# Kernel tuning notes

Hardware: AMD Instinct MI355X
Metric: run time of the kernel (lower is better)

Reference implementation:

```python
import jax, jax.numpy as jnp
import numpy as np

B, C, D = 32, 24, 12          # batch, feature channels, spatial grid
Q_DIM = 11                    # hardcoded question dim in original (k*2+11)
K = C + 2                     # channels after coordinate concat
G_IN = 2 * K + Q_DIM          # 63
G_HID = 256
F_OUT = 10


def setup_inputs() -> dict:
    key = jax.random.key(0)
    ks = jax.random.split(key, 7)
    s = lambda fan_in: 1.0 / np.sqrt(fan_in)
    return {
        "image": jax.random.normal(ks[0], (B, C, D, D), jnp.float32),
        "question": jax.random.normal(ks[1], (B, Q_DIM), jnp.float32),
        "Wg1": jax.random.normal(ks[2], (G_IN, G_HID), jnp.float32) * s(G_IN),
        "bg1": jnp.zeros((G_HID,), jnp.float32),
        "Wg2": jax.random.normal(ks[3], (G_HID, G_HID), jnp.float32) * s(G_HID),
        "bg2": jnp.zeros((G_HID,), jnp.float32),
        "Wf1": jax.random.normal(ks[4], (G_HID, G_HID), jnp.float32) * s(G_HID),
        "bf1": jnp.zeros((G_HID,), jnp.float32),
        "Wf2": jax.random.normal(ks[5], (G_HID, F_OUT), jnp.float32) * s(G_HID),
        "bf2": jnp.zeros((F_OUT,), jnp.float32),
    }


def reference(image, question, Wg1, bg1, Wg2, bg2, Wf1, bf1, Wf2, bf2):
    b, c, d, _ = image.shape
    # coordinate channels: torch.arange(0, 1+1e-5, 1/(d-1)) == linspace(0,1,d)
    coord = jnp.linspace(0.0, 1.0, d, dtype=image.dtype)
    cx = jnp.broadcast_to(coord[None, None, None, :], (b, 1, d, d))
    cy = jnp.broadcast_to(coord[None, None, :, None], (b, 1, d, d))
    x = jnp.concatenate([image, cx, cy], axis=1)            # [b, k, d, d]
    k = c + 2
    n = d * d
    x = x.reshape(b, k, n).transpose(0, 2, 1)                # [b, n, k] objects
    # all-pairs construction: left repeats objects along axis 1, right along axis 2
    x_left = jnp.broadcast_to(x[:, None, :, :], (b, n, n, k)).reshape(b, n * n, k)
    x_right = jnp.broadcast_to(x[:, :, None, :], (b, n, n, k)).reshape(b, n * n, k)
    q = jnp.broadcast_to(question[:, None, :], (b, n * n, question.shape[1]))
    pairs = jnp.concatenate([x_left, x_right, q], axis=2)    # [b, n^2, 2k+11]
    # shared MLP g per pair
    h = jax.nn.relu(jnp.einsum('bpi,ih->bph', pairs, Wg1) + bg1)
    h = jax.nn.relu(jnp.einsum('bph,ho->bpo', h, Wg2) + bg2)
    s = h.sum(axis=1)                                        # [b, 256] sum over pairs
    # MLP f
    o = jax.nn.relu(s @ Wf1 + bf1)
    return o @ Wf2 + bf2                                     # [b, 10]
```

## Files before the change

kernel.cpp:

```cpp
#include <hip/hip_runtime.h>
#include <hip/hip_bf16.h>

#define NB   32
#define NC   24
#define ND   12
#define NN   144
#define QD   11
#define GH   256
#define FOUT 10

typedef unsigned short u16;
typedef __attribute__((ext_vector_type(8))) short bf16x8;
typedef __attribute__((ext_vector_type(4))) float f32x4;

#define LQ_U16  0
#define R_U16   1179648
#define BS_U16  2359296
#define S_BYTE  4849664

__device__ inline float b2f(u16 v) {
  union { unsigned u; float f; } c; c.u = ((unsigned)v) << 16; return c.f;
}
__device__ inline u16 f2b(float f) {
  __hip_bfloat16 h = __float2bfloat16(f);
  return *reinterpret_cast<u16*>(&h);
}

__global__ __launch_bounds__(256) void prep(const float* __restrict__ image,
                                            const float* __restrict__ question,
                                            const float* __restrict__ Wg1,
                                            const float* __restrict__ bg1,
                                            const float* __restrict__ Wg2,
                                            u16* __restrict__ Lq,
                                            u16* __restrict__ R,
                                            float* __restrict__ S,
                                            u16* __restrict__ Bswz) {
  int blk = blockIdx.x;
  int h   = threadIdx.x;
  if (blk < 256) {
    const int quarter = blk & 3;
    const int b       = (blk >> 2) & 31;
    const int which   = blk >> 7;
    float Wl[NC + 2];
#pragma unroll
    for (int r = 0; r < NC + 2; ++r)
      Wl[r] = Wg1[(which * (NC + 2) + r) * GH + h];
    float qacc = 0.f;
    if (which == 0) {
      qacc = bg1[h];
#pragma unroll
      for (int tq = 0; tq < QD; ++tq)
        qacc += question[b * QD + tq] * Wg1[(2 * (NC + 2) + tq) * GH + h];
    }
    const float* img = image + b * (NC * NN);
    u16* dst = (which == 0 ? Lq : R) + b * NN * GH + h;
    const float inv = 1.0f / (ND - 1);
#pragma unroll 4
    for (int p = quarter * 36; p < quarter * 36 + 36; ++p) {
      float acc = qacc;
#pragma unroll
      for (int c = 0; c < NC; ++c) acc += img[c * NN + p] * Wl[c];
      int i = p / ND, j = p - i * ND;
      acc += (j * inv) * Wl[24];
      acc += (i * inv) * Wl[25];
      dst[p * GH] = f2b(acc);
    }
  } else {
    int tid = (blk - 256) * 256 + h;
    int e   = tid & 7;
    int l   = (tid >> 3) & 63;
    int fid = tid >> 9;
    int kt  = fid >> 4, nt = fid & 15;
    int k = kt * 32 + ((l >> 4) << 3) + e;
    int n = (nt << 4) + (l & 15);
    Bswz[tid] = f2b(Wg2[k * GH + n]);
    if (tid < NB * GH) S[tid] = 0.f;
  }
}

__global__ __launch_bounds__(512, 2) void pair_gemm(const u16* __restrict__ Lq,
                                                    const u16* __restrict__ R,
                                                    const u16* __restrict__ Bswz,
                                                    const float* __restrict__ bg2,
                                                    float* __restrict__ S) {
  const int bid = blockIdx.x;
  const int xcd = bid & 7;
  const int idx = bid >> 3;
  const int b   = xcd * 4 + (idx >> 4);
  const int bi  = idx & 15;
  const int t0  = bi * 10 + (bi < 2 ? bi : 2);
  const int cnt = 10 + (bi < 2 ? 1 : 0);

  if (idx & 32) __builtin_amdgcn_s_sleep(94);

  __shared__ __align__(16) u16 As[8 * 8 * 64 * 8];

  const int t = threadIdx.x;
  const int w = t >> 6, l = t & 63;
  const int wn = w & 3, wm = w >> 2;
  const int brow = t >> 2;
  const int oc   = t & 3;
  const int mf_w   = brow >> 4;
  const int lane_w = ((brow & 15) | (oc << 4)) ^ (oc << 1);
  const int lane_r = l ^ (((l >> 4) & 3) << 1);

  const u16* Lbase = Lq + b * NN * GH;
  const u16* Rbase = R + b * NN * GH;
  const u16* Bl    = Bswz + l * 8;

  float bgv[4];
#pragma unroll
  for (int nt = 0; nt < 4; ++nt)
    bgv[nt] = bg2[(wn << 6) + (nt << 4) + (l & 15)];
  float ssum[4] = {0.f, 0.f, 0.f, 0.f};

  for (int tt = 0; tt < cnt; ++tt) {
    {
      int p = (t0 + tt) * 128 + brow;
      int i = p / NN, j = p - i * NN;
      const u16* Lr = Lbase + i * GH + oc * 8;
      const u16* Rr = Rbase + j * GH + oc * 8;
#pragma unroll
      for (int half = 0; half < 2; ++half) {
        bf16x8 lv[4], rv[4];
#pragma unroll
        for (int q = 0; q < 4; ++q) {
          lv[q] = *(const bf16x8*)(Lr + ((half << 2) | q) * 32);
          rv[q] = *(const bf16x8*)(Rr + ((half << 2) | q) * 32);
        }
#pragma unroll
        for (int q = 0; q < 4; ++q) {
          const int kt = (half << 2) | q;
          u16 o[8];
#pragma unroll
          for (int e = 0; e < 8; ++e) {
            float v = b2f((u16)lv[q][e]) + b2f((u16)rv[q][e]);
            o[e] = f2b(v > 0.f ? v : 0.f);
          }
          *(bf16x8*)&As[((((kt << 3) | mf_w) << 6) | lane_w) << 3] =
              *(bf16x8*)o;
        }
      }
    }
    __syncthreads();

    f32x4 acc[4][4] = {};
#pragma unroll
    for (int kt = 0; kt < 8; ++kt) {
      bf16x8 af[4];
#pragma unroll
      for (int mf = 0; mf < 4; ++mf)
        af[mf] = *(const bf16x8*)
            &As[((((kt << 3) | (wm << 2) | mf) << 6) | lane_r) << 3];
      bf16x8 bfr[4];
#pragma unroll
      for (int nt = 0; nt < 4; ++nt) {
        int fid = (kt << 4) | (wn << 2) | nt;
        bfr[nt] = *(const bf16x8*)(Bl + ((size_t)fid << 9));
      }
      __builtin_amdgcn_s_setprio(1);
#pragma unroll
      for (int mf = 0; mf < 4; ++mf)
#pragma unroll
        for (int nt = 0; nt < 4; ++nt)
          acc[mf][nt] = __builtin_amdgcn_mfma_f32_16x16x32_bf16(
              af[mf], bfr[nt], acc[mf][nt], 0, 0, 0);
      __builtin_amdgcn_s_setprio(0);
    }
#pragma unroll
    for (int nt = 0; nt < 4; ++nt) {
      float s = 0.f;
#pragma unroll
      for (int mf = 0; mf < 4; ++mf)
#pragma unroll
        for (int r = 0; r < 4; ++r) {
          float v = acc[mf][nt][r] + bgv[nt];
          s += v > 0.f ? v : 0.f;
        }
      ssum[nt] += s;
    }
    __syncthreads();
  }

  float* Sb = S + b * GH;
#pragma unroll
  for (int nt = 0; nt < 4; ++nt) {
    float s = ssum[nt];
    s += __shfl_xor(s, 16, 64);
    s += __shfl_xor(s, 32, 64);
    if (l < 16) atomicAdd(&Sb[(wn << 6) + (nt << 4) + l], s);
  }
}

__global__ __launch_bounds__(256) void final_mlp(const float* __restrict__ S,
                                                 const float* __restrict__ Wf1,
                                                 const float* __restrict__ bf1,
                                                 const float* __restrict__ Wf2,
                                                 const float* __restrict__ bf2,
                                                 float* __restrict__ out) {
  __shared__ float sS[GH];
  __shared__ float oS[GH];
  int b = blockIdx.x, h = threadIdx.x;
  sS[h] = S[b * GH + h];
  __syncthreads();
  float acc = bf1[h];
#pragma unroll 8
  for (int k = 0; k < GH; ++k) acc += sS[k] * Wf1[k * GH + h];
  oS[h] = acc > 0.f ? acc : 0.f;
  __syncthreads();
  if (h < FOUT) {
    float o = bf2[h];
#pragma unroll 8
    for (int k = 0; k < GH; ++k) o += oS[k] * Wf2[k * FOUT + h];
    out[b * FOUT + h] = o;
  }
}

extern "C" void kernel_launch(void* const* d_in, const int* in_sizes, int n_in,
                              void* d_out, int out_size, void* d_ws, size_t ws_size,
                              hipStream_t stream) {
  const float* image    = (const float*)d_in[0];
  const float* question = (const float*)d_in[1];
  const float* Wg1      = (const float*)d_in[2];
  const float* bg1      = (const float*)d_in[3];
  const float* Wg2      = (const float*)d_in[4];
  const float* bg2      = (const float*)d_in[5];
  const float* Wf1      = (const float*)d_in[6];
  const float* bf1      = (const float*)d_in[7];
  const float* Wf2      = (const float*)d_in[8];
  const float* bf2      = (const float*)d_in[9];
  float* out = (float*)d_out;

  u16*   wsb  = (u16*)d_ws;
  u16*   Lqp  = wsb + LQ_U16;
  u16*   Rp   = wsb + R_U16;
  u16*   Bswz = wsb + BS_U16;
  float* Sp   = (float*)((char*)d_ws + S_BYTE);

  prep<<<512, 256, 0, stream>>>(image, question, Wg1, bg1, Wg2,
                                Lqp, Rp, Sp, Bswz);
  pair_gemm<<<512, 512, 0, stream>>>(Lqp, Rp, Bswz, bg2, Sp);
  final_mlp<<<NB, 256, 0, stream>>>(Sp, Wf1, bf1, Wf2, bf2, out);
}
```

Baseline: 110.6 us.

## Warp-specialize pair GEMM into producer and MFMA consumer waves with double-buffered LDS

Splits each block into four producer waves and four consumer waves. The producers build the relu(L+R) A tile into a double-buffered LDS buffer while the consumers run MFMA on the other buffer, each consumer covering 128 rows by 64 columns. The grid is halved to 256 blocks with twice the tiles per block, and the sleep staggering and priority hints are removed. The aim is to overlap A-tile construction with matrix math. The trade-off is fewer resident blocks, doubled LDS per block, and only half the waves issuing MFMA.

```diff
diff --git a/kernel.cpp b/kernel.cpp
--- a/kernel.cpp
+++ b/kernel.cpp
@@ -78,7 +78,7 @@
   }
 }
 
-__global__ __launch_bounds__(512, 2) void pair_gemm(const u16* __restrict__ Lq,
+__global__ __launch_bounds__(512, 1) void pair_gemm(const u16* __restrict__ Lq,
                                                     const u16* __restrict__ R,
                                                     const u16* __restrict__ Bswz,
                                                     const float* __restrict__ bg2,
@@ -86,109 +86,133 @@
   const int bid = blockIdx.x;
   const int xcd = bid & 7;
   const int idx = bid >> 3;
-  const int b   = xcd * 4 + (idx >> 4);
-  const int bi  = idx & 15;
-  const int t0  = bi * 10 + (bi < 2 ? bi : 2);
-  const int cnt = 10 + (bi < 2 ? 1 : 0);
-
-  if (idx & 32) __builtin_amdgcn_s_sleep(94);
-
-  __shared__ __align__(16) u16 As[8 * 8 * 64 * 8];
+  const int b   = xcd * 4 + (idx >> 3);
+  const int bi  = idx & 7;
+  const int t0  = bi * 20 + (bi < 2 ? bi : 2);
+  const int cnt = 20 + (bi < 2 ? 1 : 0);
+
+  __shared__ __align__(16) u16 As[2][32768];
 
   const int t = threadIdx.x;
   const int w = t >> 6, l = t & 63;
-  const int wn = w & 3, wm = w >> 2;
-  const int brow = t >> 2;
-  const int oc   = t & 3;
-  const int mf_w   = brow >> 4;
-  const int lane_w = ((brow & 15) | (oc << 4)) ^ (oc << 1);
-  const int lane_r = l ^ (((l >> 4) & 3) << 1);
 
   const u16* Lbase = Lq + b * NN * GH;
   const u16* Rbase = R + b * NN * GH;
-  const u16* Bl    = Bswz + l * 8;
-
-  float bgv[4];
-#pragma unroll
-  for (int nt = 0; nt < 4; ++nt)
-    bgv[nt] = bg2[(wn << 6) + (nt << 4) + (l & 15)];
-  float ssum[4] = {0.f, 0.f, 0.f, 0.f};
-
-  for (int tt = 0; tt < cnt; ++tt) {
+
+  if (w >= 4) {
+    const int tl    = t & 255;
+    const int row   = tl >> 1;
+    const int khalf = tl & 1;
+    const int mf_w  = row >> 4;
+
     {
-      int p = (t0 + tt) * 128 + brow;
+      int p = t0 * 128 + row;
       int i = p / NN, j = p - i * NN;
-      const u16* Lr = Lbase + i * GH + oc * 8;
-      const u16* Rr = Rbase + j * GH + oc * 8;
-#pragma unroll
-      for (int half = 0; half < 2; ++half) {
-        bf16x8 lv[4], rv[4];
-#pragma unroll
-        for (int q = 0; q < 4; ++q) {
-          lv[q] = *(const bf16x8*)(Lr + ((half << 2) | q) * 32);
-          rv[q] = *(const bf16x8*)(Rr + ((half << 2) | q) * 32);
-        }
-#pragma unroll
-        for (int q = 0; q < 4; ++q) {
-          const int kt = (half << 2) | q;
+      const u16* Lr = Lbase + i * GH + khalf * 128;
+      const u16* Rr = Rbase + j * GH + khalf * 128;
+#pragma unroll
+      for (int u = 0; u < 16; ++u) {
+        bf16x8 lv = *(const bf16x8*)(Lr + u * 8);
+        bf16x8 rv = *(const bf16x8*)(Rr + u * 8);
+        u16 o[8];
+#pragma unroll
+        for (int e = 0; e < 8; ++e) {
+          float v = b2f((u16)lv[e]) + b2f((u16)rv[e]);
+          o[e] = f2b(v > 0.f ? v : 0.f);
+        }
+        const int kt = (khalf << 2) + (u >> 2);
+        const int oc = u & 3;
+        const int lw = ((row & 15) | (oc << 4)) ^ (oc << 1);
+        *(bf16x8*)&As[0][((((kt << 3) | mf_w) << 6) | lw) << 3] = *(bf16x8*)o;
+      }
+    }
+    __syncthreads();
+
+    int cur = 0;
+    for (int tt = 0; tt < cnt; ++tt) {
+      if (tt + 1 < cnt) {
+        int p = (t0 + tt + 1) * 128 + row;
+        int i = p / NN, j = p - i * NN;
+        const u16* Lr = Lbase + i * GH + khalf * 128;
+        const u16* Rr = Rbase + j * GH + khalf * 128;
+        u16* dst = &As[cur ^ 1][0];
+#pragma unroll
+        for (int u = 0; u < 16; ++u) {
+          bf16x8 lv = *(const bf16x8*)(Lr + u * 8);
+          bf16x8 rv = *(const bf16x8*)(Rr + u * 8);
           u16 o[8];
 #pragma unroll
           for (int e = 0; e < 8; ++e) {
-            float v = b2f((u16)lv[q][e]) + b2f((u16)rv[q][e]);
+            float v = b2f((u16)lv[e]) + b2f((u16)rv[e]);
             o[e] = f2b(v > 0.f ? v : 0.f);
           }
-          *(bf16x8*)&As[((((kt << 3) | mf_w) << 6) | lane_w) << 3] =
-              *(bf16x8*)o;
-        }
-      }
-    }
+          const int kt = (khalf << 2) + (u >> 2);
+          const int oc = u & 3;
+          const int lw = ((row & 15) | (oc << 4)) ^ (oc << 1);
+          *(bf16x8*)&dst[((((kt << 3) | mf_w) << 6) | lw) << 3] = *(bf16x8*)o;
+        }
+      }
+      __syncthreads();
+      cur ^= 1;
+    }
+  } else {
+    const int lane_r = l ^ (((l >> 4) & 3) << 1);
+    const u16* Bl = Bswz + l * 8;
+
+    float bgv[4];
+#pragma unroll
+    for (int nt = 0; nt < 4; ++nt)
+      bgv[nt] = bg2[(w << 6) + (nt << 4) + (l & 15)];
+    float ssum[4] = {0.f, 0.f, 0.f, 0.f};
+
     __syncthreads();
 
-    f32x4 acc[4][4] = {};
-#pragma unroll
-    for (int kt = 0; kt < 8; ++kt) {
-      bf16x8 af[4];
-#pragma unroll
-      for (int mf = 0; mf < 4; ++mf)
-        af[mf] = *(const bf16x8*)
-            &As[((((kt << 3) | (wm << 2) | mf) << 6) | lane_r) << 3];
-      bf16x8 bfr[4];
+    int cur = 0;
+    for (int tt = 0; tt < cnt; ++tt) {
+      const u16* src = &As[cur][0];
+      f32x4 acc[8][4] = {};
+#pragma unroll
+      for (int kt = 0; kt < 8; ++kt) {
+        bf16x8 bfr[4];
+#pragma unroll
+        for (int nt = 0; nt < 4; ++nt) {
+          int fid = (kt << 4) | (w << 2) | nt;
+          bfr[nt] = *(const bf16x8*)(Bl + ((size_t)fid << 9));
+        }
+#pragma unroll
+        for (int mf = 0; mf < 8; ++mf) {
+          bf16x8 af = *(const bf16x8*)
+              &src[((((kt << 3) | mf) << 6) | lane_r) << 3];
+#pragma unroll
+          for (int nt = 0; nt < 4; ++nt)
+            acc[mf][nt] = __builtin_amdgcn_mfma_f32_16x16x32_bf16(
+                af, bfr[nt], acc[mf][nt], 0, 0, 0);
+        }
+      }
 #pragma unroll
       for (int nt = 0; nt < 4; ++nt) {
-        int fid = (kt << 4) | (wn << 2) | nt;
-        bfr[nt] = *(const bf16x8*)(Bl + ((size_t)fid << 9));
-      }
-      __builtin_amdgcn_s_setprio(1);
-#pragma unroll
-      for (int mf = 0; mf < 4; ++mf)
-#pragma unroll
-        for (int nt = 0; nt < 4; ++nt)
-          acc[mf][nt] = __builtin_amdgcn_mfma_f32_16x16x32_bf16(
-              af[mf], bfr[nt], acc[mf][nt], 0, 0, 0);
-      __builtin_amdgcn_s_setprio(0);
-    }
+        float s = 0.f;
+#pragma unroll
+        for (int mf = 0; mf < 8; ++mf)
+#pragma unroll
+          for (int r = 0; r < 4; ++r) {
+            float v = acc[mf][nt][r] + bgv[nt];
+            s += v > 0.f ? v : 0.f;
+          }
+        ssum[nt] += s;
+      }
+      __syncthreads();
+      cur ^= 1;
+    }
+
+    float* Sb = S + b * GH;
 #pragma unroll
     for (int nt = 0; nt < 4; ++nt) {
-      float s = 0.f;
-#pragma unroll
-      for (int mf = 0; mf < 4; ++mf)
-#pragma unroll
-        for (int r = 0; r < 4; ++r) {
-          float v = acc[mf][nt][r] + bgv[nt];
-          s += v > 0.f ? v : 0.f;
-        }
-      ssum[nt] += s;
-    }
-    __syncthreads();
-  }
-
-  float* Sb = S + b * GH;
-#pragma unroll
-  for (int nt = 0; nt < 4; ++nt) {
-    float s = ssum[nt];
-    s += __shfl_xor(s, 16, 64);
-    s += __shfl_xor(s, 32, 64);
-    if (l < 16) atomicAdd(&Sb[(wn << 6) + (nt << 4) + l], s);
+      float s = ssum[nt];
+      s += __shfl_xor(s, 16, 64);
+      s += __shfl_xor(s, 32, 64);
+      if (l < 16) atomicAdd(&Sb[(w << 6) + (nt << 4) + l], s);
+    }
   }
 }
 
@@ -239,6 +263,6 @@
 
   prep<<<512, 256, 0, stream>>>(image, question, Wg1, bg1, Wg2,
                                 Lqp, Rp, Sp, Bswz);
-  pair_gemm<<<512, 512, 0, stream>>>(Lqp, Rp, Bswz, bg2, Sp);
+  pair_gemm<<<256, 512, 0, stream>>>(Lqp, Rp, Bswz, bg2, Sp);
   final_mlp<<<NB, 256, 0, stream>>>(Sp, Wf1, bf1, Wf2, bf2, out);
 }
```

Result: slower. 176.9 us (+59.9%).
